# Optimization experiments

Measured on AMD Instinct MI355X. Metric: run time of the kernel, lower is better.

The kernel has to match this reference:

```python
import jax, jax.numpy as jnp
import numpy as np

EMBED_DIM = 1024
NUM_HEADS = 16
HEAD_DIM = EMBED_DIM // NUM_HEADS


def setup_inputs() -> dict:
    key = jax.random.key(0)
    ks = jax.random.split(key, 9)
    B, T, C = 2, 2048, EMBED_DIM
    s = 1.0 / np.sqrt(C)
    return {
        "x": jax.random.normal(ks[0], (B, T, C), dtype=jnp.float32),
        "Wq": jax.random.normal(ks[1], (C, C), dtype=jnp.float32) * s,
        "bq": jnp.zeros((C,), dtype=jnp.float32),
        "Wk": jax.random.normal(ks[2], (C, C), dtype=jnp.float32) * s,
        "bk": jnp.zeros((C,), dtype=jnp.float32),
        "Wv": jax.random.normal(ks[3], (C, C), dtype=jnp.float32) * s,
        "bv": jnp.zeros((C,), dtype=jnp.float32),
        "Wo": jax.random.normal(ks[4], (C, C), dtype=jnp.float32) * s,
        "bo": jnp.zeros((C,), dtype=jnp.float32),
    }


def reference(x, Wq, bq, Wk, bk, Wv, bv, Wo, bo):
    B, T, C = x.shape
    H, D = NUM_HEADS, HEAD_DIM
    # projections (torch Linear: x @ W.T + b; here W stored as [in,out])
    q = (x @ Wq + bq).reshape(B, T, H, D).transpose(0, 2, 1, 3)  # [B,H,T,D]
    k = (x @ Wk + bk).reshape(B, T, H, D).transpose(0, 2, 1, 3)
    v = (x @ Wv + bv).reshape(B, T, H, D).transpose(0, 2, 1, 3)
    scores = jnp.einsum("bhtd,bhsd->bhts", q, k) / jnp.sqrt(jnp.float32(D))
    causal = jnp.tril(jnp.ones((T, T), dtype=bool))  # keep lower triangle
    scores = jnp.where(causal, scores, -jnp.inf)
    weights = jax.nn.softmax(scores, axis=-1)
    attended = jnp.einsum("bhts,bhsd->bhtd", weights, v)
    attended = attended.transpose(0, 2, 1, 3).reshape(B, T, C)
    return attended @ Wo + bo
```

## Files before the change

kernel.cpp:

```cpp
#include <hip/hip_runtime.h>
#include <math.h>


#define BLOCK 256

typedef __attribute__((ext_vector_type(8))) short bf16x8;
typedef __attribute__((ext_vector_type(4))) float f32x4;
typedef __attribute__((ext_vector_type(16))) float f32x16;

__device__ inline short f2bf(float f) {
  union { float f; unsigned u; } c; c.f = f;
  unsigned u = c.u;
  unsigned r = (u + 0x7fffu + ((u >> 16) & 1u)) >> 16;
  return (short)r;
}

#define GLD_LDS16(g, l)                                            \
  __builtin_amdgcn_global_load_lds(                                \
      (const __attribute__((address_space(1))) unsigned int*)(g),  \
      (__attribute__((address_space(3))) unsigned int*)(l), 16, 0, 0)


__global__ void cvt_all_kernel(const float* __restrict__ x,
                               const float* __restrict__ Wq, const float* __restrict__ Wk,
                               const float* __restrict__ Wv, const float* __restrict__ Wo,
                               short* __restrict__ xb,
                               short* __restrict__ Wtqkv, short* __restrict__ Wto) {
  int z = blockIdx.z;
  if (z >= 4) {
    int blk = blockIdx.x + (blockIdx.y << 5) + ((z - 4) << 10);
    int i = (blk * 256 + threadIdx.x) * 8;
    float4 a = *(const float4*)(x + i);
    float4 b = *(const float4*)(x + i + 4);
    alignas(16) short o[8];
    o[0] = f2bf(a.x); o[1] = f2bf(a.y); o[2] = f2bf(a.z); o[3] = f2bf(a.w);
    o[4] = f2bf(b.x); o[5] = f2bf(b.y); o[6] = f2bf(b.z); o[7] = f2bf(b.w);
    *(int4*)(xb + i) = *(int4*)o;
    return;
  }
  __shared__ float tile[32][33];
  const float* W = (z == 0) ? Wq : (z == 1) ? Wk : (z == 2) ? Wv : Wo;
  short* outp = (z == 3) ? Wto : (Wtqkv + (size_t)z * 1024 * 1024);
  int k0 = blockIdx.x * 32, n0 = blockIdx.y * 32;
  int tr = threadIdx.x >> 5, tc = threadIdx.x & 31;
#pragma unroll
  for (int i = 0; i < 4; i++)
    tile[tr + i * 8][tc] = W[(k0 + tr + i * 8) * 1024 + n0 + tc];
  __syncthreads();
#pragma unroll
  for (int i = 0; i < 4; i++)
    outp[(n0 + tr + i * 8) * 1024 + k0 + tc] = f2bf(tile[tc][tr + i * 8]);
}


__global__ __launch_bounds__(BLOCK, 3) void gemm_qkv_kernel(
    const short* __restrict__ A, const short* __restrict__ Wt,
    const float* __restrict__ bq, const float* __restrict__ bk,
    const float* __restrict__ bv,
    short* __restrict__ Qo, short* __restrict__ Ko, short* __restrict__ Vo) {
  const int Kd = 1024;
  const float QSCL = 0.18033688011f;
  int p = blockIdx.x;
  int xcd = p & 7, j = p >> 3;
  int m0 = ((xcd & 3) * 8 + (j & 7)) * 128;
  int n0 = ((xcd >> 2) * 12 + (j >> 3)) * 128;
  int t = threadIdx.x;
  int lane = t & 63, wv = t >> 6;
  int quad = lane >> 4, lc = lane & 15;
  int wy = wv >> 1, wx = wv & 1;
  __shared__ short As[128 * 64];
  __shared__ short Bs[128 * 64];
  f32x4 acc[4][4] = {};

  int sr = wv * 32 + (lane >> 3);
  int schk = lane & 7;
  const short* Ab = A + (size_t)(m0 + sr) * Kd + schk * 8;
  const short* Bb = Wt + (size_t)(n0 + sr) * Kd + schk * 8;
  int wslot = schk ^ (lane >> 3);
  short* wa = &As[sr * 64 + wslot * 8];
  short* wb = &Bs[sr * 64 + wslot * 8];

  bf16x8 sA[4], sB[4];
#pragma unroll
  for (int i = 0; i < 4; i++) {
    sA[i] = *(const bf16x8*)(Ab + (size_t)(i * 8) * Kd);
    sB[i] = *(const bf16x8*)(Bb + (size_t)(i * 8) * Kd);
  }
  int rx = lc & 7;
  for (int step = 0; step < 16; step++) {
#pragma unroll
    for (int i = 0; i < 4; i++) {
      *(bf16x8*)(wa + i * 8 * 64) = sA[i];
      *(bf16x8*)(wb + i * 8 * 64) = sB[i];
    }
    asm volatile("s_waitcnt lgkmcnt(0)" ::: "memory");
    __builtin_amdgcn_s_barrier();
    asm volatile("" ::: "memory");
    if (step + 1 < 16) {
      int koff = (step + 1) * 64;
#pragma unroll
      for (int i = 0; i < 4; i++) {
        sA[i] = *(const bf16x8*)(Ab + (size_t)(i * 8) * Kd + koff);
        sB[i] = *(const bf16x8*)(Bb + (size_t)(i * 8) * Kd + koff);
      }
    }
#pragma unroll
    for (int kc = 0; kc < 2; kc++) {
      bf16x8 af[4], bf[4];
#pragma unroll
      for (int i = 0; i < 4; i++)
        af[i] = *(const bf16x8*)&As[(wy * 64 + i * 16 + lc) * 64 +
                                    ((kc * 4 + quad) ^ rx) * 8];
#pragma unroll
      for (int i = 0; i < 4; i++)
        bf[i] = *(const bf16x8*)&Bs[(wx * 64 + i * 16 + lc) * 64 +
                                    ((kc * 4 + quad) ^ rx) * 8];
#pragma unroll
      for (int mi = 0; mi < 4; mi++)
#pragma unroll
        for (int ni = 0; ni < 4; ni++)
          acc[mi][ni] = __builtin_amdgcn_mfma_f32_16x16x32_bf16(af[mi], bf[ni], acc[mi][ni], 0, 0, 0);
    }
    asm volatile("s_waitcnt lgkmcnt(0)" ::: "memory");
    __builtin_amdgcn_s_barrier();
    asm volatile("" ::: "memory");
  }
#pragma unroll
  for (int mi = 0; mi < 4; mi++) {
    int row = m0 + wy * 64 + mi * 16 + quad * 4;
#pragma unroll
    for (int ni = 0; ni < 4; ni++) {
      int col = n0 + wx * 64 + ni * 16 + lc;
      int which = col >> 10;
      int hd = col & 1023;
      int h = hd >> 6, d = hd & 63;
      float bb = (which == 0) ? bq[hd] : (which == 1) ? bk[hd] : bv[hd];
      if (which == 2) {
        alignas(8) short pk[4];
#pragma unroll
        for (int r = 0; r < 4; r++) pk[r] = f2bf(acc[mi][ni][r] + bb);
        int b = row >> 11, tt = row & 2047;
        *(int2*)&Vo[((size_t)(b * 16 + h) * 64 + d) * 2048 + tt] = *(const int2*)pk;
      } else {
#pragma unroll
        for (int r = 0; r < 4; r++) {
          int rw = row + r;
          int b = rw >> 11, tt = rw & 2047;
          float val = acc[mi][ni][r] + bb;
          if (which == 0) {
            Qo[((size_t)(b * 16 + h) * 2048 + tt) * 64 + d] = f2bf(val * QSCL);
          } else {
            Ko[((size_t)(b * 16 + h) * 2048 + tt) * 64 + d] = f2bf(val);
          }
        }
      }
    }
  }
}


__global__ __launch_bounds__(BLOCK) void gemm_out_kernel(
    const short* __restrict__ A, const short* __restrict__ Wt,
    const float* __restrict__ bias, float* __restrict__ Out) {
  const int Kd = 1024;
  int m0 = blockIdx.x * 64, n0 = blockIdx.y * 128;
  int t = threadIdx.x;
  int lane = t & 63, wv = t >> 6;
  int quad = lane >> 4, lc = lane & 15;
  int wy = wv >> 1, wx = wv & 1;
  __shared__ short As[2][64 * 32];
  __shared__ short Bs[2][128 * 32];
  int r0 = t >> 2, c0 = (t & 3) * 8;
  f32x4 acc[2][4] = {};
  const short* Arow0 = A + (size_t)(m0 + r0) * Kd + c0;
  const short* Brow0 = Wt + (size_t)(n0 + r0) * Kd + c0;
  const short* Brow1 = Wt + (size_t)(n0 + r0 + 64) * Kd + c0;
  GLD_LDS16(Arow0, &As[0][8 * t]);
  GLD_LDS16(Brow0, &Bs[0][8 * t]);
  GLD_LDS16(Brow1, &Bs[0][8 * t + 2048]);
  int cur = 0;
  for (int k0 = 0; k0 < Kd; k0 += 32) {
    __syncthreads();
    if (k0 + 32 < Kd) {
      int nxt = cur ^ 1;
      GLD_LDS16(Arow0 + k0 + 32, &As[nxt][8 * t]);
      GLD_LDS16(Brow0 + k0 + 32, &Bs[nxt][8 * t]);
      GLD_LDS16(Brow1 + k0 + 32, &Bs[nxt][8 * t + 2048]);
    }
    bf16x8 af[2], bf[4];
#pragma unroll
    for (int i = 0; i < 2; i++)
      af[i] = *(const bf16x8*)&As[cur][(wy * 32 + i * 16 + lc) * 32 + quad * 8];
#pragma unroll
    for (int i = 0; i < 4; i++)
      bf[i] = *(const bf16x8*)&Bs[cur][(wx * 64 + i * 16 + lc) * 32 + quad * 8];
#pragma unroll
    for (int mi = 0; mi < 2; mi++)
#pragma unroll
      for (int ni = 0; ni < 4; ni++)
        acc[mi][ni] = __builtin_amdgcn_mfma_f32_16x16x32_bf16(af[mi], bf[ni], acc[mi][ni], 0, 0, 0);
    cur ^= 1;
  }
#pragma unroll
  for (int mi = 0; mi < 2; mi++) {
    int row = m0 + wy * 32 + mi * 16 + quad * 4;
#pragma unroll
    for (int ni = 0; ni < 4; ni++) {
      int col = n0 + wx * 64 + ni * 16 + lc;
      float bb = bias[col];
#pragma unroll
      for (int r = 0; r < 4; r++)
        Out[(size_t)(row + r) * 1024 + col] = acc[mi][ni][r] + bb;
    }
  }
}


__global__ __launch_bounds__(BLOCK, 2) void attn_kernel(
    const short* __restrict__ Q, const short* __restrict__ K,
    const short* __restrict__ Vt, short* __restrict__ Oa) {
  int p = blockIdx.x;
  int bh = ((p & 7) << 2) | ((p >> 3) & 3);
  int pair = p >> 5;
  int t = threadIdx.x;
  int lane = t & 63, w = t >> 6;
  int qh = w & 1, kh = w >> 1;
  int ln = lane & 31, lh = lane >> 5;
  const short* Qb = Q + (size_t)bh * 2048 * 64;
  const short* Kb = K + (size_t)bh * 2048 * 64;
  const short* Vg = Vt + (size_t)bh * 64 * 2048;
  int b = bh >> 4, h = bh & 15;

  __shared__ short Kt[2][64 * 64];
  __shared__ short Vs[2][64 * 64];
  __shared__ __align__(16) short Ps[4][32 * 72];
  __shared__ float lx[2][64];
  short* Pw = Ps[w];

  int srow = t >> 3;
  int sw = t & 7;
  const float M2 = 14.5f;
  int xk = ln & 7;

  for (int sp = 0; sp < 2; sp++) {
    int s = sp ? (31 - pair) : pair;
    int q0 = s * 64;
    int q0w = q0 + qh * 32;
    int qmaxw = q0w + 31;
    int ntiles = s + 1;

    bf16x8 qf[4];
#pragma unroll
    for (int c = 0; c < 4; c++)
      qf[c] = *(const bf16x8*)&Qb[(size_t)(q0w + ln) * 64 + c * 16 + lh * 8];

    f32x16 O0 = {}, O1 = {};
    float lsum = 0.f;

#pragma unroll
    for (int i = 0; i < 2; i++) {
      int r = i * 32 + srow;
      int cg = sw ^ (r & 7);
      GLD_LDS16(&Kb[(size_t)r * 64 + cg * 8], &Kt[0][i * 2048 + 8 * t]);
      GLD_LDS16(&Vg[(size_t)r * 2048 + cg * 8], &Vs[0][i * 2048 + 8 * t]);
    }
    int cur = 0;
    for (int kt = 0; kt < ntiles; kt++) {
      __syncthreads();
      if (kt + 1 < ntiles) {
        int kb2 = (kt + 1) * 64;
        int nxt = cur ^ 1;
#pragma unroll
        for (int i = 0; i < 2; i++) {
          int r = i * 32 + srow;
          int cg = sw ^ (r & 7);
          GLD_LDS16(&Kb[(size_t)(kb2 + r) * 64 + cg * 8], &Kt[nxt][i * 2048 + 8 * t]);
          GLD_LDS16(&Vg[(size_t)r * 2048 + kb2 + cg * 8], &Vs[nxt][i * 2048 + 8 * t]);
        }
      }
      int grpbase = kt * 64 + kh * 32;
      if (grpbase <= qmaxw) {
        f32x16 S = {};
#pragma unroll
        for (int c = 0; c < 4; c++) {
          int ch = c * 2 + lh;
          bf16x8 kf = *(const bf16x8*)&Kt[cur][(kh * 32 + ln) * 64 + (ch ^ xk) * 8];
          S = __builtin_amdgcn_mfma_f32_32x32x16_bf16(kf, qf[c], S, 0, 0, 0);
        }
        if (kt == ntiles - 1) {
          int qg = q0w + ln;
#pragma unroll
          for (int reg = 0; reg < 16; reg++) {
            int key = grpbase + (reg & 3) + 8 * (reg >> 2) + 4 * lh;
            if (key > qg) S[reg] = -3.0e38f;
          }
        }
#pragma unroll
        for (int g = 0; g < 4; g++) {
          unsigned u[4];
#pragma unroll
          for (int i = 0; i < 4; i++) {
            union { float f; unsigned v; } cc;
            cc.f = __builtin_amdgcn_exp2f(S[g * 4 + i] - M2);
            lsum += cc.f;
            u[i] = cc.v + 0x8000u;
          }
          int2 pk;
          pk.x = (int)__builtin_amdgcn_perm(u[1], u[0], 0x07060302);
          pk.y = (int)__builtin_amdgcn_perm(u[3], u[2], 0x07060302);
          *(int2*)&Pw[ln * 72 + g * 8 + lh * 4] = pk;
        }
#pragma unroll
        for (int c2 = 0; c2 < 2; c2++) {
          bf16x8 pf = *(const bf16x8*)&Pw[ln * 72 + c2 * 16 + lh * 8];
          int ch = kh * 4 + c2 * 2 + lh;
          bf16x8 v0 = *(const bf16x8*)&Vs[cur][ln * 64 + (ch ^ xk) * 8];
          bf16x8 v1 = *(const bf16x8*)&Vs[cur][(32 + ln) * 64 + (ch ^ xk) * 8];
          O0 = __builtin_amdgcn_mfma_f32_32x32x16_bf16(v0, pf, O0, 0, 0, 0);
          O1 = __builtin_amdgcn_mfma_f32_32x32x16_bf16(v1, pf, O1, 0, 0, 0);
        }
      }
      cur ^= 1;
    }

    float* ob = (float*)&Ps[0][0];
    __syncthreads();
    if (kh == 1) {
      float* obw = ob + qh * 2048;
#pragma unroll
      for (int dh = 0; dh < 2; dh++)
#pragma unroll
        for (int reg = 0; reg < 16; reg++)
          obw[((dh * 16 + reg) * 2 + lh) * 32 + ln] = dh ? O1[reg] : O0[reg];
      lx[qh][lane] = lsum;
    }
    __syncthreads();
    if (kh == 0) {
      float* obw = ob + qh * 2048;
#pragma unroll
      for (int reg = 0; reg < 16; reg++) {
        O0[reg] += obw[((0 * 16 + reg) * 2 + lh) * 32 + ln];
        O1[reg] += obw[((1 * 16 + reg) * 2 + lh) * 32 + ln];
      }
      float lt = lsum + lx[qh][lane];
      lt += __shfl_xor(lt, 32, 64);
      float inv = 1.0f / lt;
      size_t rowbase = (size_t)(b * 2048 + q0w + ln) * 1024 + h * 64;
#pragma unroll
      for (int dh = 0; dh < 2; dh++)
#pragma unroll
        for (int g = 0; g < 4; g++) {
          alignas(8) short pk[4];
#pragma unroll
          for (int i = 0; i < 4; i++) {
            float v = dh ? O1[g * 4 + i] : O0[g * 4 + i];
            pk[i] = f2bf(v * inv);
          }
          *(int2*)&Oa[rowbase + dh * 32 + g * 8 + lh * 4] = *(const int2*)pk;
        }
    }
  }
}


extern "C" void kernel_launch(void* const* d_in, const int* in_sizes, int n_in,
                              void* d_out, int out_size, void* d_ws, size_t ws_size,
                              hipStream_t stream) {
  const float* x = (const float*)d_in[0];
  const float* Wq = (const float*)d_in[1];
  const float* bq = (const float*)d_in[2];
  const float* Wk = (const float*)d_in[3];
  const float* bk = (const float*)d_in[4];
  const float* Wv = (const float*)d_in[5];
  const float* bv = (const float*)d_in[6];
  const float* Wo = (const float*)d_in[7];
  const float* bo = (const float*)d_in[8];
  char* ws = (char*)d_ws;
  const size_t MB = 1024 * 1024;
  short* xb = (short*)(ws);
  short* Wtqkv = (short*)(ws + 8 * MB);
  short* Wto = (short*)(ws + 14 * MB);
  short* Qb = (short*)(ws + 17 * MB);
  short* Kb = (short*)(ws + 25 * MB);
  short* Vb = (short*)(ws + 33 * MB);
  short* Att = (short*)(ws + 41 * MB);
  float* out = (float*)d_out;

  cvt_all_kernel<<<dim3(32, 32, 6), BLOCK, 0, stream>>>(x, Wq, Wk, Wv, Wo, xb, Wtqkv, Wto);
  gemm_qkv_kernel<<<dim3(768), BLOCK, 0, stream>>>(xb, Wtqkv, bq, bk, bv, Qb, Kb, Vb);
  attn_kernel<<<512, BLOCK, 0, stream>>>(Qb, Kb, Vb, Att);
  gemm_out_kernel<<<dim3(64, 8), BLOCK, 0, stream>>>(Att, Wto, bo, out);
}
```

Baseline: 178.3 us.

## Replace direct global-to-LDS loads with register-staged prefetch in GEMM and attention

Both the output-projection GEMM and the attention kernel drop the global_load_lds double-buffered path. They now prefetch the next tile into registers while computing on a single LDS buffer, which is written with an XOR-swizzled layout between barriers. The GEMM also widens its K step from 32 to 64 per iteration, halving the number of barrier rounds. This halves LDS usage and may allow higher occupancy, at the cost of extra VGPRs and two barriers per iteration instead of one.

```diff
diff --git a/kernel.cpp b/kernel.cpp
--- a/kernel.cpp
+++ b/kernel.cpp
@@ -14,11 +14,6 @@
   unsigned r = (u + 0x7fffu + ((u >> 16) & 1u)) >> 16;
   return (short)r;
 }
-
-#define GLD_LDS16(g, l)                                            \
-  __builtin_amdgcn_global_load_lds(                                \
-      (const __attribute__((address_space(1))) unsigned int*)(g),  \
-      (__attribute__((address_space(3))) unsigned int*)(l), 16, 0, 0)
 
 
 __global__ void cvt_all_kernel(const float* __restrict__ x,
@@ -168,38 +163,64 @@
   int lane = t & 63, wv = t >> 6;
   int quad = lane >> 4, lc = lane & 15;
   int wy = wv >> 1, wx = wv & 1;
-  __shared__ short As[2][64 * 32];
-  __shared__ short Bs[2][128 * 32];
-  int r0 = t >> 2, c0 = (t & 3) * 8;
+  __shared__ short As[64 * 64];
+  __shared__ short Bs[128 * 64];
   f32x4 acc[2][4] = {};
-  const short* Arow0 = A + (size_t)(m0 + r0) * Kd + c0;
-  const short* Brow0 = Wt + (size_t)(n0 + r0) * Kd + c0;
-  const short* Brow1 = Wt + (size_t)(n0 + r0 + 64) * Kd + c0;
-  GLD_LDS16(Arow0, &As[0][8 * t]);
-  GLD_LDS16(Brow0, &Bs[0][8 * t]);
-  GLD_LDS16(Brow1, &Bs[0][8 * t + 2048]);
-  int cur = 0;
-  for (int k0 = 0; k0 < Kd; k0 += 32) {
-    __syncthreads();
-    if (k0 + 32 < Kd) {
-      int nxt = cur ^ 1;
-      GLD_LDS16(Arow0 + k0 + 32, &As[nxt][8 * t]);
-      GLD_LDS16(Brow0 + k0 + 32, &Bs[nxt][8 * t]);
-      GLD_LDS16(Brow1 + k0 + 32, &Bs[nxt][8 * t + 2048]);
-    }
-    bf16x8 af[2], bf[4];
-#pragma unroll
-    for (int i = 0; i < 2; i++)
-      af[i] = *(const bf16x8*)&As[cur][(wy * 32 + i * 16 + lc) * 32 + quad * 8];
-#pragma unroll
-    for (int i = 0; i < 4; i++)
-      bf[i] = *(const bf16x8*)&Bs[cur][(wx * 64 + i * 16 + lc) * 32 + quad * 8];
-#pragma unroll
-    for (int mi = 0; mi < 2; mi++)
-#pragma unroll
-      for (int ni = 0; ni < 4; ni++)
-        acc[mi][ni] = __builtin_amdgcn_mfma_f32_16x16x32_bf16(af[mi], bf[ni], acc[mi][ni], 0, 0, 0);
-    cur ^= 1;
+
+  int lr = lane >> 3;
+  int schk = lane & 7;
+  int wslot = schk ^ lr;
+  int srA = wv * 16 + lr;
+  int srB = wv * 32 + lr;
+  const short* Ab = A + (size_t)(m0 + srA) * Kd + schk * 8;
+  const short* Bb = Wt + (size_t)(n0 + srB) * Kd + schk * 8;
+  short* wa = &As[srA * 64 + wslot * 8];
+  short* wb = &Bs[srB * 64 + wslot * 8];
+
+  bf16x8 sA[2], sB[4];
+#pragma unroll
+  for (int i = 0; i < 2; i++) sA[i] = *(const bf16x8*)(Ab + (size_t)(i * 8) * Kd);
+#pragma unroll
+  for (int i = 0; i < 4; i++) sB[i] = *(const bf16x8*)(Bb + (size_t)(i * 8) * Kd);
+
+  int rx = lc & 7;
+  for (int step = 0; step < 16; step++) {
+#pragma unroll
+    for (int i = 0; i < 2; i++) *(bf16x8*)(wa + i * 8 * 64) = sA[i];
+#pragma unroll
+    for (int i = 0; i < 4; i++) *(bf16x8*)(wb + i * 8 * 64) = sB[i];
+    asm volatile("s_waitcnt lgkmcnt(0)" ::: "memory");
+    __builtin_amdgcn_s_barrier();
+    asm volatile("" ::: "memory");
+    if (step + 1 < 16) {
+      int koff = (step + 1) * 64;
+#pragma unroll
+      for (int i = 0; i < 2; i++)
+        sA[i] = *(const bf16x8*)(Ab + (size_t)(i * 8) * Kd + koff);
+#pragma unroll
+      for (int i = 0; i < 4; i++)
+        sB[i] = *(const bf16x8*)(Bb + (size_t)(i * 8) * Kd + koff);
+    }
+#pragma unroll
+    for (int kc = 0; kc < 2; kc++) {
+      bf16x8 af[2], bf[4];
+#pragma unroll
+      for (int i = 0; i < 2; i++)
+        af[i] = *(const bf16x8*)&As[(wy * 32 + i * 16 + lc) * 64 +
+                                    ((kc * 4 + quad) ^ rx) * 8];
+#pragma unroll
+      for (int i = 0; i < 4; i++)
+        bf[i] = *(const bf16x8*)&Bs[(wx * 64 + i * 16 + lc) * 64 +
+                                    ((kc * 4 + quad) ^ rx) * 8];
+#pragma unroll
+      for (int mi = 0; mi < 2; mi++)
+#pragma unroll
+        for (int ni = 0; ni < 4; ni++)
+          acc[mi][ni] = __builtin_amdgcn_mfma_f32_16x16x32_bf16(af[mi], bf[ni], acc[mi][ni], 0, 0, 0);
+    }
+    asm volatile("s_waitcnt lgkmcnt(0)" ::: "memory");
+    __builtin_amdgcn_s_barrier();
+    asm volatile("" ::: "memory");
   }
 #pragma unroll
   for (int mi = 0; mi < 2; mi++) {
@@ -231,14 +252,15 @@
   const short* Vg = Vt + (size_t)bh * 64 * 2048;
   int b = bh >> 4, h = bh & 15;
 
-  __shared__ short Kt[2][64 * 64];
-  __shared__ short Vs[2][64 * 64];
+  __shared__ short Kt[64 * 64];
+  __shared__ short Vs[64 * 64];
   __shared__ __align__(16) short Ps[4][32 * 72];
   __shared__ float lx[2][64];
   short* Pw = Ps[w];
 
   int srow = t >> 3;
-  int sw = t & 7;
+  int schk = t & 7;
+  int wslot = (schk ^ (srow & 7)) * 8;
   const float M2 = 14.5f;
   int xk = ln & 7;
 
@@ -257,25 +279,30 @@
     f32x16 O0 = {}, O1 = {};
     float lsum = 0.f;
 
+    bf16x8 sK[2], sV[2];
 #pragma unroll
     for (int i = 0; i < 2; i++) {
       int r = i * 32 + srow;
-      int cg = sw ^ (r & 7);
-      GLD_LDS16(&Kb[(size_t)r * 64 + cg * 8], &Kt[0][i * 2048 + 8 * t]);
-      GLD_LDS16(&Vg[(size_t)r * 2048 + cg * 8], &Vs[0][i * 2048 + 8 * t]);
-    }
-    int cur = 0;
+      sK[i] = *(const bf16x8*)&Kb[(size_t)r * 64 + schk * 8];
+      sV[i] = *(const bf16x8*)&Vg[(size_t)r * 2048 + schk * 8];
+    }
     for (int kt = 0; kt < ntiles; kt++) {
-      __syncthreads();
+#pragma unroll
+      for (int i = 0; i < 2; i++) {
+        int r = i * 32 + srow;
+        *(bf16x8*)&Kt[r * 64 + wslot] = sK[i];
+        *(bf16x8*)&Vs[r * 64 + wslot] = sV[i];
+      }
+      asm volatile("s_waitcnt lgkmcnt(0)" ::: "memory");
+      __builtin_amdgcn_s_barrier();
+      asm volatile("" ::: "memory");
       if (kt + 1 < ntiles) {
         int kb2 = (kt + 1) * 64;
-        int nxt = cur ^ 1;
 #pragma unroll
         for (int i = 0; i < 2; i++) {
           int r = i * 32 + srow;
-          int cg = sw ^ (r & 7);
-          GLD_LDS16(&Kb[(size_t)(kb2 + r) * 64 + cg * 8], &Kt[nxt][i * 2048 + 8 * t]);
-          GLD_LDS16(&Vg[(size_t)r * 2048 + kb2 + cg * 8], &Vs[nxt][i * 2048 + 8 * t]);
+          sK[i] = *(const bf16x8*)&Kb[(size_t)(kb2 + r) * 64 + schk * 8];
+          sV[i] = *(const bf16x8*)&Vg[(size_t)r * 2048 + kb2 + schk * 8];
         }
       }
       int grpbase = kt * 64 + kh * 32;
@@ -284,7 +311,7 @@
 #pragma unroll
         for (int c = 0; c < 4; c++) {
           int ch = c * 2 + lh;
-          bf16x8 kf = *(const bf16x8*)&Kt[cur][(kh * 32 + ln) * 64 + (ch ^ xk) * 8];
+          bf16x8 kf = *(const bf16x8*)&Kt[(kh * 32 + ln) * 64 + (ch ^ xk) * 8];
           S = __builtin_amdgcn_mfma_f32_32x32x16_bf16(kf, qf[c], S, 0, 0, 0);
         }
         if (kt == ntiles - 1) {
@@ -314,17 +341,18 @@
         for (int c2 = 0; c2 < 2; c2++) {
           bf16x8 pf = *(const bf16x8*)&Pw[ln * 72 + c2 * 16 + lh * 8];
           int ch = kh * 4 + c2 * 2 + lh;
-          bf16x8 v0 = *(const bf16x8*)&Vs[cur][ln * 64 + (ch ^ xk) * 8];
-          bf16x8 v1 = *(const bf16x8*)&Vs[cur][(32 + ln) * 64 + (ch ^ xk) * 8];
+          bf16x8 v0 = *(const bf16x8*)&Vs[ln * 64 + (ch ^ xk) * 8];
+          bf16x8 v1 = *(const bf16x8*)&Vs[(32 + ln) * 64 + (ch ^ xk) * 8];
           O0 = __builtin_amdgcn_mfma_f32_32x32x16_bf16(v0, pf, O0, 0, 0, 0);
           O1 = __builtin_amdgcn_mfma_f32_32x32x16_bf16(v1, pf, O1, 0, 0, 0);
         }
       }
-      cur ^= 1;
+      asm volatile("s_waitcnt lgkmcnt(0)" ::: "memory");
+      __builtin_amdgcn_s_barrier();
+      asm volatile("" ::: "memory");
     }
 
     float* ob = (float*)&Ps[0][0];
-    __syncthreads();
     if (kh == 1) {
       float* obw = ob + qh * 2048;
 #pragma unroll
```

New measurement: 171.5 us. 3.8% less time.
